# Kernel tuning notes

Hardware: AMD Instinct MI355X
Metric: run time of the kernel (lower is better)

Reference implementation:

```python
import jax, jax.numpy as jnp
import numpy as np

RSQRT2 = 2 ** (-0.5)
B, S, D_IN = 2, 4096, 1024
H, D_HEAD = 8, 64            # num_heads, attention_dim (per-head qk and v dim)
QK_DIM = H * D_HEAD          # 512
V_DIM = H * D_HEAD           # 512
OUT_DIM = D_IN               # 1024 (output_dim defaults to input_dim)
LN_EPS = 1e-5


def setup_inputs() -> dict:
    key = jax.random.key(0)
    ks = jax.random.split(key, 8)
    def lecun(k, fan_in, shape):
        return jax.random.normal(k, shape, dtype=jnp.float32) * (1.0 / np.sqrt(fan_in))
    return {
        "x": jax.random.normal(ks[0], (B, S, D_IN), dtype=jnp.float32),
        # weights stored [in, out] (transposed torch Linear layout)
        "W_qk": lecun(ks[1], D_IN, (D_IN, 2 * QK_DIM)),
        "b_qk": jnp.zeros((2 * QK_DIM,), jnp.float32),
        "W_v": lecun(ks[2], D_IN, (D_IN, V_DIM)),
        "b_v": jnp.zeros((V_DIM,), jnp.float32),
        "W_out": lecun(ks[3], V_DIM, (V_DIM, OUT_DIM)),
        "b_out": jnp.zeros((OUT_DIM,), jnp.float32),
        "ln_gamma": jnp.ones((OUT_DIM,), jnp.float32),
        "ln_beta": jnp.zeros((OUT_DIM,), jnp.float32),
    }


def _layernorm(y, gamma, beta):
    mu = jnp.mean(y, axis=-1, keepdims=True)
    var = jnp.mean(jnp.square(y - mu), axis=-1, keepdims=True)
    return (y - mu) * jax.lax.rsqrt(var + LN_EPS) * gamma + beta


def reference(x, W_qk, b_qk, W_v, b_v, W_out, b_out, ln_gamma, ln_beta):
    b, s, _ = x.shape
    scale = D_HEAD ** (-0.5)
    qk = x @ W_qk + b_qk                          # [b, s, 2*h*d]
    qk = qk.reshape(b, s, H, D_HEAD, 2)           # c (q/k) is fastest axis
    q, k = qk[..., 0], qk[..., 1]                 # [b, s, h, d]
    v = (x @ W_v + b_v).reshape(b, s, H, D_HEAD)  # [b, s, h, d]
    # manual multi-head attention, full O(s^2) score matrix (as in source)
    sim = jnp.einsum("bihd,bjhd->bhij", q, k) * scale
    attn = jax.nn.softmax(sim, axis=-1)           # [b, h, i, j]
    o = jnp.einsum("bhij,bjhd->bihd", attn, v)    # [b, s, h, d]
    o = o.reshape(b, s, V_DIM)                    # 'b h s d -> b s (h d)'
    y = _layernorm(o @ W_out + b_out, ln_gamma, ln_beta)
    return (y + x) * RSQRT2
```

## Files before the change

kernel.cpp:

```cpp
#include <hip/hip_runtime.h>
#include <stdint.h>

typedef short bf16x8 __attribute__((ext_vector_type(8)));
typedef float f32x4 __attribute__((ext_vector_type(4)));
typedef unsigned short ushort_t;

#define RSQRT2_F 0.70710678118654752440f
#define QSCALE_F 0.18033688011114382f

__device__ __forceinline__ ushort_t f2bf(float f) {
  union { float f; uint32_t u; } c; c.f = f;
  uint32_t u = c.u;
  uint32_t r = (u + 0x7fffu + ((u >> 16) & 1u)) >> 16;
  return (ushort_t)r;
}
__device__ __forceinline__ float bf2f(ushort_t u) {
  union { uint32_t u; float f; } c; c.u = ((uint32_t)u) << 16;
  return c.f;
}
__device__ __forceinline__ uint32_t fbits(float f) {
  union { float f; uint32_t u; } c; c.f = f; return c.u;
}

__device__ __forceinline__ void gload_lds16(const void* g, void* l) {
  __builtin_amdgcn_global_load_lds(
      (const __attribute__((address_space(1))) void*)g,
      (__attribute__((address_space(3))) void*)l, 16, 0, 0);
}

__global__ __launch_bounds__(256) void k_cvt_x(const float* __restrict__ x,
                                               ushort_t* __restrict__ xb) {
  int i = (blockIdx.x * 256 + threadIdx.x) * 4;
  float4 f = *(const float4*)(x + i);
  ushort4 o;
  o.x = f2bf(f.x); o.y = f2bf(f.y); o.z = f2bf(f.z); o.w = f2bf(f.w);
  *(ushort4*)(xb + i) = o;
}

__global__ __launch_bounds__(256) void k_build_wqkv(const float* __restrict__ Wqk,
                                                    const float* __restrict__ bqk,
                                                    const float* __restrict__ Wv,
                                                    const float* __restrict__ bv,
                                                    ushort_t* __restrict__ Wt,
                                                    float* __restrict__ biasAll) {
  int k = blockIdx.x * 256 + threadIdx.x;
  int n = blockIdx.y;
  float w, bb;
  if (n < 512)       { w = Wqk[(size_t)k * 1024 + 2 * n] * QSCALE_F;     bb = bqk[2 * n] * QSCALE_F; }
  else if (n < 1024) { w = Wqk[(size_t)k * 1024 + 2 * (n - 512) + 1];    bb = bqk[2 * (n - 512) + 1]; }
  else               { w = Wv[(size_t)k * 512 + (n - 1024)];             bb = bv[n - 1024]; }
  Wt[(size_t)n * 1024 + k] = f2bf(w);
  if (k == 0) biasAll[n] = bb;
}

__global__ __launch_bounds__(256) void k_build_wout(const float* __restrict__ Wout,
                                                    ushort_t* __restrict__ Wt) {
  int k = blockIdx.x * 256 + threadIdx.x;
  int n = blockIdx.y;
  Wt[(size_t)n * 512 + k] = f2bf(Wout[(size_t)k * 1024 + n]);
}

template <int MODE>
__global__ __launch_bounds__(256) void k_gemm_bt(
    const ushort_t* __restrict__ A, const ushort_t* __restrict__ Bt,
    const float* __restrict__ bias,
    ushort_t* __restrict__ out0, ushort_t* __restrict__ out1, ushort_t* __restrict__ out2,
    int M, int N, int K) {
  __shared__ __align__(16) ushort_t As[4][128][8];
  __shared__ __align__(16) ushort_t Bs[4][128][8];
  const int t = threadIdx.x;
  const int lane = t & 63;
  const int wave = t >> 6;
  const int m0 = blockIdx.x * 128, n0 = blockIdx.y * 128;
  const int wm = (wave >> 1) * 64, wn = (wave & 1) * 64;
  const int lg = lane >> 4, lr = lane & 15;

  const int srow = t & 127, sg = t >> 7;
  ushort_t* lA0 = &As[sg][srow][0];
  ushort_t* lA1 = &As[sg + 2][srow][0];
  ushort_t* lB0 = &Bs[sg][srow][0];
  ushort_t* lB1 = &Bs[sg + 2][srow][0];
  const ushort_t* gA = A + (size_t)(m0 + srow) * K + sg * 8;
  const ushort_t* gB = Bt + (size_t)(n0 + srow) * K + sg * 8;

  f32x4 acc[4][4] = {};

  for (int k0 = 0; k0 < K; k0 += 32) {
    __syncthreads();
    gload_lds16(gA + k0, lA0);
    gload_lds16(gA + k0 + 16, lA1);
    gload_lds16(gB + k0, lB0);
    gload_lds16(gB + k0 + 16, lB1);
    __syncthreads();
    bf16x8 af[4], bfr[4];
#pragma unroll
    for (int mi = 0; mi < 4; mi++) af[mi] = *(const bf16x8*)&As[lg][wm + mi * 16 + lr][0];
#pragma unroll
    for (int ni = 0; ni < 4; ni++) bfr[ni] = *(const bf16x8*)&Bs[lg][wn + ni * 16 + lr][0];
#pragma unroll
    for (int mi = 0; mi < 4; mi++)
#pragma unroll
      for (int ni = 0; ni < 4; ni++)
        acc[mi][ni] = __builtin_amdgcn_mfma_f32_16x16x32_bf16(af[mi], bfr[ni], acc[mi][ni], 0, 0, 0);
  }

#pragma unroll
  for (int mi = 0; mi < 4; mi++) {
    int rowb = m0 + wm + mi * 16 + (lane >> 4) * 4;
#pragma unroll
    for (int ni = 0; ni < 4; ni++) {
      int col = n0 + wn + ni * 16 + lr;
      float bc = bias[col];
#pragma unroll
      for (int reg = 0; reg < 4; reg++) {
        int row = rowb + reg;
        float v = acc[mi][ni][reg] + bc;
        if (MODE == 0) {
          if (col < 512) {
            out0[(size_t)row * 512 + col] = f2bf(v);
          } else if (col < 1024) {
            out1[(size_t)row * 512 + (col - 512)] = f2bf(v);
          } else {
            int hd = col - 1024;
            int bb = row >> 12, s = row & 4095;
            out2[((size_t)(bb << 9) + hd) * 4096 + s] = f2bf(v);
          }
        } else {
          out0[(size_t)row * 1024 + col] = f2bf(v);
        }
      }
    }
  }
}

__global__ __launch_bounds__(128) void k_attn(const ushort_t* __restrict__ Qb,
                                              const ushort_t* __restrict__ Kb,
                                              const ushort_t* __restrict__ Vt,
                                              ushort_t* __restrict__ Ob) {
  __shared__ __align__(16) ushort_t Ks[8][64][8];
  __shared__ __align__(16) ushort_t Vs[8][64][8];
  __shared__ __align__(16) ushort_t Pl[4][1024];
  const int S = 4096, HD = 512;
  const int t = threadIdx.x, lane = t & 63, wave = t >> 6;
  const int lg = lane >> 4, lr = lane & 15;

  const int bid = blockIdx.x;
  const int xcd = bid & 7, idx = bid >> 3;
  const int bh = (xcd << 1) | (idx >> 6);
  const int qb = idx & 63;
  const int b = bh >> 3, h = bh & 7;
  const int qbase = qb * 64 + wave * 32;

  bf16x8 qf[2][2];
#pragma unroll
  for (int su = 0; su < 2; su++) {
    const ushort_t* qp = Qb + ((size_t)(b * S + qbase + su * 16 + lr)) * HD + h * 64 + lg * 8;
    qf[su][0] = *(const bf16x8*)qp;
    qf[su][1] = *(const bf16x8*)(qp + 32);
  }

  const int sj = t & 63;
  const ushort_t* gK = Kb + ((size_t)b * S + sj) * HD + h * 64 + wave * 8;
  const ushort_t* gV = Vt + ((size_t)bh * 64 + sj) * S + wave * 8;
  ushort_t* lK = &Ks[wave][sj][0];
  ushort_t* lV = &Vs[wave][sj][0];

  char* Pbase = (char*)&Pl[wave * 2][0];

  const bf16x8 vones = {(short)0x3F80, (short)0x3F80, (short)0x3F80, (short)0x3F80,
                        (short)0x3F80, (short)0x3F80, (short)0x3F80, (short)0x3F80};

  f32x4 of[2][4] = {};
  f32x4 of_sum[2] = {};
  float m_run[2] = {-1e30f, -1e30f};

  for (int kv0 = 0; kv0 < S; kv0 += 64) {
    __syncthreads();
#pragma unroll
    for (int i = 0; i < 4; i++) {
      gload_lds16(gK + (size_t)kv0 * HD + i * 16, lK + i * 1024);
      gload_lds16(gV + kv0 + i * 16, lV + i * 1024);
    }
    __syncthreads();

    f32x4 sf[2][4];
#pragma unroll
    for (int nt = 0; nt < 4; nt++) {
      bf16x8 kf0 = *(const bf16x8*)&Ks[lg][nt * 16 + lr][0];
      bf16x8 kf1 = *(const bf16x8*)&Ks[4 + lg][nt * 16 + lr][0];
#pragma unroll
      for (int su = 0; su < 2; su++) {
        f32x4 z = {};
        z = __builtin_amdgcn_mfma_f32_16x16x32_bf16(kf0, qf[su][0], z, 0, 0, 0);
        sf[su][nt] = __builtin_amdgcn_mfma_f32_16x16x32_bf16(kf1, qf[su][1], z, 0, 0, 0);
      }
    }

#pragma unroll
    for (int su = 0; su < 2; su++) {
      float pmax = sf[su][0][0];
#pragma unroll
      for (int nt = 0; nt < 4; nt++)
#pragma unroll
        for (int r = 0; r < 4; r++) pmax = fmaxf(pmax, sf[su][nt][r]);
      pmax = fmaxf(pmax, __shfl_xor(pmax, 16, 64));
      pmax = fmaxf(pmax, __shfl_xor(pmax, 32, 64));

      if (__any(pmax > m_run[su] + 11.0f)) {
        float mnew = fmaxf(m_run[su], pmax);
        float scl = __builtin_amdgcn_exp2f(m_run[su] - mnew);
        m_run[su] = mnew;
        float sclr[4];
#pragma unroll
        for (int r = 0; r < 4; r++) sclr[r] = __shfl(scl, lg * 4 + r, 64);
#pragma unroll
        for (int dt = 0; dt < 4; dt++)
#pragma unroll
          for (int r = 0; r < 4; r++) of[su][dt][r] *= sclr[r];
#pragma unroll
        for (int r = 0; r < 4; r++) of_sum[su][r] *= sclr[r];
      }

      char* Pb = Pbase + su * 2048;
#pragma unroll
      for (int nt = 0; nt < 4; nt++) {
        float p0 = __builtin_amdgcn_exp2f(sf[su][nt][0] - m_run[su]);
        float p1 = __builtin_amdgcn_exp2f(sf[su][nt][1] - m_run[su]);
        float p2 = __builtin_amdgcn_exp2f(sf[su][nt][2] - m_run[su]);
        float p3 = __builtin_amdgcn_exp2f(sf[su][nt][3] - m_run[su]);
        uint32_t w0 = (fbits(p0) >> 16) | (fbits(p1) & 0xffff0000u);
        uint32_t w1 = (fbits(p2) >> 16) | (fbits(p3) & 0xffff0000u);
        int off = (lr * 128 + nt * 32 + lg * 8) ^ ((lr & 7) << 4);
        *(uint2*)(Pb + off) = make_uint2(w0, w1);
      }
    }

    bf16x8 pf[2][2];
#pragma unroll
    for (int su = 0; su < 2; su++)
#pragma unroll
      for (int kc = 0; kc < 2; kc++) {
        int off = (lr * 128 + kc * 64 + lg * 16) ^ ((lr & 7) << 4);
        pf[su][kc] = *(const bf16x8*)(Pbase + su * 2048 + off);
      }

#pragma unroll
    for (int dt = 0; dt < 4; dt++) {
      bf16x8 vf0 = *(const bf16x8*)&Vs[lg][dt * 16 + lr][0];
      bf16x8 vf1 = *(const bf16x8*)&Vs[4 + lg][dt * 16 + lr][0];
#pragma unroll
      for (int su = 0; su < 2; su++) {
        of[su][dt] = __builtin_amdgcn_mfma_f32_16x16x32_bf16(pf[su][0], vf0, of[su][dt], 0, 0, 0);
        of[su][dt] = __builtin_amdgcn_mfma_f32_16x16x32_bf16(pf[su][1], vf1, of[su][dt], 0, 0, 0);
      }
    }
#pragma unroll
    for (int su = 0; su < 2; su++) {
      of_sum[su] = __builtin_amdgcn_mfma_f32_16x16x32_bf16(pf[su][0], vones, of_sum[su], 0, 0, 0);
      of_sum[su] = __builtin_amdgcn_mfma_f32_16x16x32_bf16(pf[su][1], vones, of_sum[su], 0, 0, 0);
    }
  }

#pragma unroll
  for (int su = 0; su < 2; su++) {
    float inv[4];
#pragma unroll
    for (int r = 0; r < 4; r++) inv[r] = 1.0f / of_sum[su][r];
#pragma unroll
    for (int dt = 0; dt < 4; dt++)
#pragma unroll
      for (int r = 0; r < 4; r++) {
        int q = qbase + su * 16 + lg * 4 + r;
        Ob[((size_t)b * S + q) * 512 + h * 64 + dt * 16 + lr] = f2bf(of[su][dt][r] * inv[r]);
      }
  }
}

__global__ __launch_bounds__(256) void k_ln(const ushort_t* __restrict__ ypre,
                                            const float* __restrict__ x,
                                            const float* __restrict__ gamma,
                                            const float* __restrict__ beta,
                                            float* __restrict__ out) {
  __shared__ float red[8];
  const int row = blockIdx.x, t = threadIdx.x;
  const ushort_t* yr = ypre + (size_t)row * 1024;
  ushort4 u = *(const ushort4*)(yr + t * 4);
  float v0 = bf2f(u.x), v1 = bf2f(u.y), v2 = bf2f(u.z), v3 = bf2f(u.w);
  float s = v0 + v1 + v2 + v3;
  float sq = v0 * v0 + v1 * v1 + v2 * v2 + v3 * v3;
#pragma unroll
  for (int m = 32; m; m >>= 1) { s += __shfl_xor(s, m, 64); sq += __shfl_xor(sq, m, 64); }
  if ((t & 63) == 0) { red[t >> 6] = s; red[4 + (t >> 6)] = sq; }
  __syncthreads();
  s = red[0] + red[1] + red[2] + red[3];
  sq = red[4] + red[5] + red[6] + red[7];
  float mu = s * (1.f / 1024.f);
  float var = sq * (1.f / 1024.f) - mu * mu;
  float inv = rsqrtf(var + 1e-5f);
  int c = t * 4;
  float4 xf = *(const float4*)(x + (size_t)row * 1024 + c);
  float4 o;
  o.x = ((v0 - mu) * inv * gamma[c + 0] + beta[c + 0] + xf.x) * RSQRT2_F;
  o.y = ((v1 - mu) * inv * gamma[c + 1] + beta[c + 1] + xf.y) * RSQRT2_F;
  o.z = ((v2 - mu) * inv * gamma[c + 2] + beta[c + 2] + xf.z) * RSQRT2_F;
  o.w = ((v3 - mu) * inv * gamma[c + 3] + beta[c + 3] + xf.w) * RSQRT2_F;
  *(float4*)(out + (size_t)row * 1024 + c) = o;
}

extern "C" void kernel_launch(void* const* d_in, const int* in_sizes, int n_in,
                              void* d_out, int out_size, void* d_ws, size_t ws_size,
                              hipStream_t stream) {
  (void)in_sizes; (void)n_in; (void)out_size; (void)ws_size;
  const float* x     = (const float*)d_in[0];
  const float* Wqk   = (const float*)d_in[1];
  const float* bqk   = (const float*)d_in[2];
  const float* Wv    = (const float*)d_in[3];
  const float* bv    = (const float*)d_in[4];
  const float* Wout  = (const float*)d_in[5];
  const float* bout  = (const float*)d_in[6];
  const float* gamma = (const float*)d_in[7];
  const float* beta  = (const float*)d_in[8];
  float* out = (float*)d_out;

  char* ws = (char*)d_ws;
  size_t off = 0;
  auto alloc = [&](size_t bytes) {
    off = (off + 255) & ~(size_t)255;
    void* p = ws + off;
    off += bytes;
    return p;
  };
  ushort_t* xb    = (ushort_t*)alloc(8192ull * 1024 * 2);
  ushort_t* Wqkvt = (ushort_t*)alloc(1536ull * 1024 * 2);
  float*    biasA = (float*)   alloc(1536ull * 4);
  ushort_t* Woutt = (ushort_t*)alloc(1024ull * 512 * 2);
  ushort_t* Qb    = (ushort_t*)alloc(8192ull * 512 * 2);
  ushort_t* Kbuf  = (ushort_t*)alloc(8192ull * 512 * 2);
  ushort_t* Vtb   = (ushort_t*)alloc(1024ull * 4096 * 2);
  ushort_t* Ob    = (ushort_t*)alloc(8192ull * 512 * 2);
  ushort_t* ypre  = xb;

  k_cvt_x<<<8192, 256, 0, stream>>>(x, xb);
  k_build_wqkv<<<dim3(4, 1536), 256, 0, stream>>>(Wqk, bqk, Wv, bv, Wqkvt, biasA);
  k_build_wout<<<dim3(2, 1024), 256, 0, stream>>>(Wout, Woutt);
  k_gemm_bt<0><<<dim3(64, 12), 256, 0, stream>>>(xb, Wqkvt, biasA, Qb, Kbuf, Vtb, 8192, 1536, 1024);
  k_attn<<<1024, 128, 0, stream>>>(Qb, Kbuf, Vtb, Ob);
  k_gemm_bt<1><<<dim3(64, 8), 256, 0, stream>>>(Ob, Woutt, bout, ypre, nullptr, nullptr, 8192, 1024, 512);
  k_ln<<<8192, 256, 0, stream>>>(ypre, x, gamma, beta, out);
}
```

Measured before the change: 247.9 us.

## Double-buffer LDS in GEMM and attention, widen attention to 4 waves, swizzle GEMM grid

Both the GEMM and attention kernels now double-buffer their LDS tiles, prefetching the next K/V or A/B tile while the current one is computed, with one barrier per iteration instead of two. The attention kernel goes from 2 waves of 32 queries each to 4 waves of 16 queries each, so each block stages K/V with more threads and holds fewer registers per wave. The GEMM launch becomes a 1D grid with an XCD-aware tile remap meant to improve L2 locality. The cost is twice the LDS per block, which may reduce occupancy.

```diff
diff --git a/kernel.cpp b/kernel.cpp
--- a/kernel.cpp
+++ b/kernel.cpp
@@ -66,43 +66,55 @@
     const float* __restrict__ bias,
     ushort_t* __restrict__ out0, ushort_t* __restrict__ out1, ushort_t* __restrict__ out2,
     int M, int N, int K) {
-  __shared__ __align__(16) ushort_t As[4][128][8];
-  __shared__ __align__(16) ushort_t Bs[4][128][8];
+  __shared__ __align__(16) ushort_t As[2][4][128][8];
+  __shared__ __align__(16) ushort_t Bs[2][4][128][8];
   const int t = threadIdx.x;
   const int lane = t & 63;
   const int wave = t >> 6;
-  const int m0 = blockIdx.x * 128, n0 = blockIdx.y * 128;
+
+  const int nby = N >> 7;
+  const int nwg = gridDim.x;
+  const int xcd = blockIdx.x & 7, pos = blockIdx.x >> 3;
+  const int swz = xcd * (nwg >> 3) + pos;
+  const int bx = swz / nby, by = swz % nby;
+  const int m0 = bx * 128, n0 = by * 128;
+
   const int wm = (wave >> 1) * 64, wn = (wave & 1) * 64;
   const int lg = lane >> 4, lr = lane & 15;
 
   const int srow = t & 127, sg = t >> 7;
-  ushort_t* lA0 = &As[sg][srow][0];
-  ushort_t* lA1 = &As[sg + 2][srow][0];
-  ushort_t* lB0 = &Bs[sg][srow][0];
-  ushort_t* lB1 = &Bs[sg + 2][srow][0];
   const ushort_t* gA = A + (size_t)(m0 + srow) * K + sg * 8;
   const ushort_t* gB = Bt + (size_t)(n0 + srow) * K + sg * 8;
 
   f32x4 acc[4][4] = {};
 
+#define GEMM_STAGE(k0, bsel)                                   \
+  do {                                                         \
+    gload_lds16(gA + (k0), &As[bsel][sg][srow][0]);            \
+    gload_lds16(gA + (k0) + 16, &As[bsel][sg + 2][srow][0]);   \
+    gload_lds16(gB + (k0), &Bs[bsel][sg][srow][0]);            \
+    gload_lds16(gB + (k0) + 16, &Bs[bsel][sg + 2][srow][0]);   \
+  } while (0)
+
+  GEMM_STAGE(0, 0);
+  __syncthreads();
+  int buf = 0;
   for (int k0 = 0; k0 < K; k0 += 32) {
-    __syncthreads();
-    gload_lds16(gA + k0, lA0);
-    gload_lds16(gA + k0 + 16, lA1);
-    gload_lds16(gB + k0, lB0);
-    gload_lds16(gB + k0 + 16, lB1);
-    __syncthreads();
+    if (k0 + 32 < K) GEMM_STAGE(k0 + 32, buf ^ 1);
     bf16x8 af[4], bfr[4];
 #pragma unroll
-    for (int mi = 0; mi < 4; mi++) af[mi] = *(const bf16x8*)&As[lg][wm + mi * 16 + lr][0];
-#pragma unroll
-    for (int ni = 0; ni < 4; ni++) bfr[ni] = *(const bf16x8*)&Bs[lg][wn + ni * 16 + lr][0];
+    for (int mi = 0; mi < 4; mi++) af[mi] = *(const bf16x8*)&As[buf][lg][wm + mi * 16 + lr][0];
+#pragma unroll
+    for (int ni = 0; ni < 4; ni++) bfr[ni] = *(const bf16x8*)&Bs[buf][lg][wn + ni * 16 + lr][0];
 #pragma unroll
     for (int mi = 0; mi < 4; mi++)
 #pragma unroll
       for (int ni = 0; ni < 4; ni++)
         acc[mi][ni] = __builtin_amdgcn_mfma_f32_16x16x32_bf16(af[mi], bfr[ni], acc[mi][ni], 0, 0, 0);
+    __syncthreads();
+    buf ^= 1;
   }
+#undef GEMM_STAGE
 
 #pragma unroll
   for (int mi = 0; mi < 4; mi++) {
@@ -133,14 +145,14 @@
   }
 }
 
-__global__ __launch_bounds__(128) void k_attn(const ushort_t* __restrict__ Qb,
-                                              const ushort_t* __restrict__ Kb,
-                                              const ushort_t* __restrict__ Vt,
-                                              ushort_t* __restrict__ Ob) {
-  __shared__ __align__(16) ushort_t Ks[8][64][8];
-  __shared__ __align__(16) ushort_t Vs[8][64][8];
+__global__ __launch_bounds__(256, 4) void k_attn(const ushort_t* __restrict__ Qb,
+                                                 const ushort_t* __restrict__ Kb,
+                                                 const ushort_t* __restrict__ Vt,
+                                                 ushort_t* __restrict__ Ob) {
+  __shared__ __align__(16) ushort_t Ks[2][8][64][8];
+  __shared__ __align__(16) ushort_t Vs[2][8][64][8];
   __shared__ __align__(16) ushort_t Pl[4][1024];
-  const int S = 4096, HD = 512;
+  const int S = 4096;
   const int t = threadIdx.x, lane = t & 63, wave = t >> 6;
   const int lg = lane >> 4, lr = lane & 15;
 
@@ -149,131 +161,117 @@
   const int bh = (xcd << 1) | (idx >> 6);
   const int qb = idx & 63;
   const int b = bh >> 3, h = bh & 7;
-  const int qbase = qb * 64 + wave * 32;
-
-  bf16x8 qf[2][2];
-#pragma unroll
-  for (int su = 0; su < 2; su++) {
-    const ushort_t* qp = Qb + ((size_t)(b * S + qbase + su * 16 + lr)) * HD + h * 64 + lg * 8;
-    qf[su][0] = *(const bf16x8*)qp;
-    qf[su][1] = *(const bf16x8*)(qp + 32);
-  }
-
-  const int sj = t & 63;
-  const ushort_t* gK = Kb + ((size_t)b * S + sj) * HD + h * 64 + wave * 8;
-  const ushort_t* gV = Vt + ((size_t)bh * 64 + sj) * S + wave * 8;
-  ushort_t* lK = &Ks[wave][sj][0];
-  ushort_t* lV = &Vs[wave][sj][0];
-
-  char* Pbase = (char*)&Pl[wave * 2][0];
+  const int qbase = qb * 64 + wave * 16;
+
+  const ushort_t* qp = Qb + ((size_t)(b * S + qbase + lr)) * 512 + h * 64 + lg * 8;
+  const bf16x8 qf0 = *(const bf16x8*)qp;
+  const bf16x8 qf1 = *(const bf16x8*)(qp + 32);
+
+  const int cj = t & 63, cg = t >> 6;
+  const ushort_t* gK = Kb + ((size_t)b * S + cj) * 512 + h * 64 + cg * 8;
+  const ushort_t* gV = Vt + ((size_t)bh * 64 + cj) * 4096 + cg * 8;
+
+  char* Pbase = (char*)&Pl[wave][0];
 
   const bf16x8 vones = {(short)0x3F80, (short)0x3F80, (short)0x3F80, (short)0x3F80,
                         (short)0x3F80, (short)0x3F80, (short)0x3F80, (short)0x3F80};
 
-  f32x4 of[2][4] = {};
-  f32x4 of_sum[2] = {};
-  float m_run[2] = {-1e30f, -1e30f};
+  f32x4 of[4] = {};
+  f32x4 of_sum = {};
+  float m_run = -1e30f;
+
+#define ATTN_STAGE(kv0, bsel)                                         \
+  do {                                                                \
+    gload_lds16(gK + (size_t)(kv0) * 512, &Ks[bsel][cg][cj][0]);      \
+    gload_lds16(gK + (size_t)(kv0) * 512 + 32, &Ks[bsel][cg + 4][cj][0]); \
+    gload_lds16(gV + (kv0), &Vs[bsel][cg][cj][0]);                    \
+    gload_lds16(gV + (kv0) + 32, &Vs[bsel][cg + 4][cj][0]);           \
+  } while (0)
+
+  ATTN_STAGE(0, 0);
+  __syncthreads();
+  int buf = 0;
 
   for (int kv0 = 0; kv0 < S; kv0 += 64) {
+    if (kv0 + 64 < S) ATTN_STAGE(kv0 + 64, buf ^ 1);
+
+    f32x4 sf[4];
+#pragma unroll
+    for (int nt = 0; nt < 4; nt++) {
+      bf16x8 kf0 = *(const bf16x8*)&Ks[buf][lg][nt * 16 + lr][0];
+      bf16x8 kf1 = *(const bf16x8*)&Ks[buf][4 + lg][nt * 16 + lr][0];
+      f32x4 z = {};
+      z = __builtin_amdgcn_mfma_f32_16x16x32_bf16(kf0, qf0, z, 0, 0, 0);
+      sf[nt] = __builtin_amdgcn_mfma_f32_16x16x32_bf16(kf1, qf1, z, 0, 0, 0);
+    }
+
+    float pmax = sf[0][0];
+#pragma unroll
+    for (int nt = 0; nt < 4; nt++)
+#pragma unroll
+      for (int r = 0; r < 4; r++) pmax = fmaxf(pmax, sf[nt][r]);
+    pmax = fmaxf(pmax, __shfl_xor(pmax, 16, 64));
+    pmax = fmaxf(pmax, __shfl_xor(pmax, 32, 64));
+
+    if (__any(pmax > m_run + 11.0f)) {
+      float mnew = fmaxf(m_run, pmax);
+      float scl = __builtin_amdgcn_exp2f(m_run - mnew);
+      m_run = mnew;
+      float sclr[4];
+#pragma unroll
+      for (int r = 0; r < 4; r++) sclr[r] = __shfl(scl, lg * 4 + r, 64);
+#pragma unroll
+      for (int dt = 0; dt < 4; dt++)
+#pragma unroll
+        for (int r = 0; r < 4; r++) of[dt][r] *= sclr[r];
+#pragma unroll
+      for (int r = 0; r < 4; r++) of_sum[r] *= sclr[r];
+    }
+
+#pragma unroll
+    for (int nt = 0; nt < 4; nt++) {
+      float p0 = __builtin_amdgcn_exp2f(sf[nt][0] - m_run);
+      float p1 = __builtin_amdgcn_exp2f(sf[nt][1] - m_run);
+      float p2 = __builtin_amdgcn_exp2f(sf[nt][2] - m_run);
+      float p3 = __builtin_amdgcn_exp2f(sf[nt][3] - m_run);
+      uint32_t w0 = (fbits(p0) >> 16) | (fbits(p1) & 0xffff0000u);
+      uint32_t w1 = (fbits(p2) >> 16) | (fbits(p3) & 0xffff0000u);
+      int off = (lr * 128 + nt * 32 + lg * 8) ^ ((lr & 7) << 4);
+      *(uint2*)(Pbase + off) = make_uint2(w0, w1);
+    }
+
+    bf16x8 pf[2];
+#pragma unroll
+    for (int kc = 0; kc < 2; kc++) {
+      int off = (lr * 128 + kc * 64 + lg * 16) ^ ((lr & 7) << 4);
+      pf[kc] = *(const bf16x8*)(Pbase + off);
+    }
+
+#pragma unroll
+    for (int dt = 0; dt < 4; dt++) {
+      bf16x8 vf0 = *(const bf16x8*)&Vs[buf][lg][dt * 16 + lr][0];
+      bf16x8 vf1 = *(const bf16x8*)&Vs[buf][4 + lg][dt * 16 + lr][0];
+      of[dt] = __builtin_amdgcn_mfma_f32_16x16x32_bf16(pf[0], vf0, of[dt], 0, 0, 0);
+      of[dt] = __builtin_amdgcn_mfma_f32_16x16x32_bf16(pf[1], vf1, of[dt], 0, 0, 0);
+    }
+    of_sum = __builtin_amdgcn_mfma_f32_16x16x32_bf16(pf[0], vones, of_sum, 0, 0, 0);
+    of_sum = __builtin_amdgcn_mfma_f32_16x16x32_bf16(pf[1], vones, of_sum, 0, 0, 0);
+
     __syncthreads();
-#pragma unroll
-    for (int i = 0; i < 4; i++) {
-      gload_lds16(gK + (size_t)kv0 * HD + i * 16, lK + i * 1024);
-      gload_lds16(gV + kv0 + i * 16, lV + i * 1024);
-    }
-    __syncthreads();
-
-    f32x4 sf[2][4];
-#pragma unroll
-    for (int nt = 0; nt < 4; nt++) {
-      bf16x8 kf0 = *(const bf16x8*)&Ks[lg][nt * 16 + lr][0];
-      bf16x8 kf1 = *(const bf16x8*)&Ks[4 + lg][nt * 16 + lr][0];
-#pragma unroll
-      for (int su = 0; su < 2; su++) {
-        f32x4 z = {};
-        z = __builtin_amdgcn_mfma_f32_16x16x32_bf16(kf0, qf[su][0], z, 0, 0, 0);
-        sf[su][nt] = __builtin_amdgcn_mfma_f32_16x16x32_bf16(kf1, qf[su][1], z, 0, 0, 0);
-      }
-    }
-
-#pragma unroll
-    for (int su = 0; su < 2; su++) {
-      float pmax = sf[su][0][0];
-#pragma unroll
-      for (int nt = 0; nt < 4; nt++)
-#pragma unroll
-        for (int r = 0; r < 4; r++) pmax = fmaxf(pmax, sf[su][nt][r]);
-      pmax = fmaxf(pmax, __shfl_xor(pmax, 16, 64));
-      pmax = fmaxf(pmax, __shfl_xor(pmax, 32, 64));
-
-      if (__any(pmax > m_run[su] + 11.0f)) {
-        float mnew = fmaxf(m_run[su], pmax);
-        float scl = __builtin_amdgcn_exp2f(m_run[su] - mnew);
-        m_run[su] = mnew;
-        float sclr[4];
-#pragma unroll
-        for (int r = 0; r < 4; r++) sclr[r] = __shfl(scl, lg * 4 + r, 64);
-#pragma unroll
-        for (int dt = 0; dt < 4; dt++)
-#pragma unroll
-          for (int r = 0; r < 4; r++) of[su][dt][r] *= sclr[r];
-#pragma unroll
-        for (int r = 0; r < 4; r++) of_sum[su][r] *= sclr[r];
-      }
-
-      char* Pb = Pbase + su * 2048;
-#pragma unroll
-      for (int nt = 0; nt < 4; nt++) {
-        float p0 = __builtin_amdgcn_exp2f(sf[su][nt][0] - m_run[su]);
-        float p1 = __builtin_amdgcn_exp2f(sf[su][nt][1] - m_run[su]);
-        float p2 = __builtin_amdgcn_exp2f(sf[su][nt][2] - m_run[su]);
-        float p3 = __builtin_amdgcn_exp2f(sf[su][nt][3] - m_run[su]);
-        uint32_t w0 = (fbits(p0) >> 16) | (fbits(p1) & 0xffff0000u);
-        uint32_t w1 = (fbits(p2) >> 16) | (fbits(p3) & 0xffff0000u);
-        int off = (lr * 128 + nt * 32 + lg * 8) ^ ((lr & 7) << 4);
-        *(uint2*)(Pb + off) = make_uint2(w0, w1);
-      }
-    }
-
-    bf16x8 pf[2][2];
-#pragma unroll
-    for (int su = 0; su < 2; su++)
-#pragma unroll
-      for (int kc = 0; kc < 2; kc++) {
-        int off = (lr * 128 + kc * 64 + lg * 16) ^ ((lr & 7) << 4);
-        pf[su][kc] = *(const bf16x8*)(Pbase + su * 2048 + off);
-      }
-
-#pragma unroll
-    for (int dt = 0; dt < 4; dt++) {
-      bf16x8 vf0 = *(const bf16x8*)&Vs[lg][dt * 16 + lr][0];
-      bf16x8 vf1 = *(const bf16x8*)&Vs[4 + lg][dt * 16 + lr][0];
-#pragma unroll
-      for (int su = 0; su < 2; su++) {
-        of[su][dt] = __builtin_amdgcn_mfma_f32_16x16x32_bf16(pf[su][0], vf0, of[su][dt], 0, 0, 0);
-        of[su][dt] = __builtin_amdgcn_mfma_f32_16x16x32_bf16(pf[su][1], vf1, of[su][dt], 0, 0, 0);
-      }
-    }
-#pragma unroll
-    for (int su = 0; su < 2; su++) {
-      of_sum[su] = __builtin_amdgcn_mfma_f32_16x16x32_bf16(pf[su][0], vones, of_sum[su], 0, 0, 0);
-      of_sum[su] = __builtin_amdgcn_mfma_f32_16x16x32_bf16(pf[su][1], vones, of_sum[su], 0, 0, 0);
-    }
+    buf ^= 1;
   }
-
-#pragma unroll
-  for (int su = 0; su < 2; su++) {
-    float inv[4];
-#pragma unroll
-    for (int r = 0; r < 4; r++) inv[r] = 1.0f / of_sum[su][r];
-#pragma unroll
-    for (int dt = 0; dt < 4; dt++)
-#pragma unroll
-      for (int r = 0; r < 4; r++) {
-        int q = qbase + su * 16 + lg * 4 + r;
-        Ob[((size_t)b * S + q) * 512 + h * 64 + dt * 16 + lr] = f2bf(of[su][dt][r] * inv[r]);
-      }
-  }
+#undef ATTN_STAGE
+
+  float inv[4];
+#pragma unroll
+  for (int r = 0; r < 4; r++) inv[r] = 1.0f / of_sum[r];
+#pragma unroll
+  for (int dt = 0; dt < 4; dt++)
+#pragma unroll
+    for (int r = 0; r < 4; r++) {
+      int q = qbase + lg * 4 + r;
+      Ob[((size_t)b * S + q) * 512 + h * 64 + dt * 16 + lr] = f2bf(of[dt][r] * inv[r]);
+    }
 }
 
 __global__ __launch_bounds__(256) void k_ln(const ushort_t* __restrict__ ypre,
@@ -343,8 +341,8 @@
   k_cvt_x<<<8192, 256, 0, stream>>>(x, xb);
   k_build_wqkv<<<dim3(4, 1536), 256, 0, stream>>>(Wqk, bqk, Wv, bv, Wqkvt, biasA);
   k_build_wout<<<dim3(2, 1024), 256, 0, stream>>>(Wout, Woutt);
-  k_gemm_bt<0><<<dim3(64, 12), 256, 0, stream>>>(xb, Wqkvt, biasA, Qb, Kbuf, Vtb, 8192, 1536, 1024);
-  k_attn<<<1024, 128, 0, stream>>>(Qb, Kbuf, Vtb, Ob);
-  k_gemm_bt<1><<<dim3(64, 8), 256, 0, stream>>>(Ob, Woutt, bout, ypre, nullptr, nullptr, 8192, 1024, 512);
+  k_gemm_bt<0><<<768, 256, 0, stream>>>(xb, Wqkvt, biasA, Qb, Kbuf, Vtb, 8192, 1536, 1024);
+  k_attn<<<1024, 256, 0, stream>>>(Qb, Kbuf, Vtb, Ob);
+  k_gemm_bt<1><<<512, 256, 0, stream>>>(Ob, Woutt, bout, ypre, nullptr, nullptr, 8192, 1024, 512);
   k_ln<<<8192, 256, 0, stream>>>(ypre, x, gamma, beta, out);
 }
```

New measurement: 247.2 us. No clear change (-0.3%).
